# Optimization experiments

Hardware: AMD Instinct MI355X
Metric: run time of the kernel (lower is better)

Reference implementation:

```python
import jax, jax.numpy as jnp
import numpy as np

N = 65536          # nodes
E = N * 7          # edges (avg_degree = n_edge_type = 7)
C_IN = 128
C_OUT = 128
N_EDGE_TYPE = 7
N_NODE_TYPE = 5
FEAT = C_IN + N_NODE_TYPE  # 133, channels after one-hot concat


def setup_inputs() -> dict:
    key = jax.random.key(0)
    k1, k2, k3, k4, k5 = jax.random.split(key, 5)
    x = jax.random.normal(k1, (N, C_IN), dtype=jnp.float32)
    edge_idx = jax.random.randint(k2, (2, E), 0, N, dtype=jnp.int64)
    edge_type = jax.random.randint(k3, (E,), 0, N_EDGE_TYPE, dtype=jnp.int64)
    node_type = jax.random.randint(k4, (N,), 0, N_NODE_TYPE, dtype=jnp.int64)
    # uniform init a la module's reset_parameters
    fan_in = 7 * C_IN
    fan_out = 7 * C_OUT
    a = np.sqrt(3.0) * np.sqrt(2.0 / (fan_in + fan_out))
    weights = jax.random.uniform(k5, (N_EDGE_TYPE * FEAT, C_OUT), dtype=jnp.float32,
                                 minval=-a, maxval=a)
    return {"x": x, "edge_idx": edge_idx, "edge_type": edge_type,
            "node_type": node_type, "weights": weights}


def reference(x, edge_idx, edge_type, node_type, weights):
    # one-hot node type concat (n_node_type > 1 branch)
    one_hot = jax.nn.one_hot(node_type, N_NODE_TYPE, dtype=x.dtype)
    xa = jnp.concatenate([x, one_hot], axis=1)          # [N, FEAT]
    row, col = edge_idx[0], edge_idx[1]
    seg = row * N_EDGE_TYPE + edge_type                 # [E]
    gathered = xa[col]                                  # [E, FEAT]
    num_seg = N * N_EDGE_TYPE
    sums = jax.ops.segment_sum(gathered, seg, num_segments=num_seg)
    cnt = jax.ops.segment_sum(jnp.ones((E,), dtype=xa.dtype), seg, num_segments=num_seg)
    col_data = sums / jnp.maximum(cnt, 1.0)[:, None]    # scatter_mean
    # overwrite self-loop slot (last edge type) with node's own features
    self_idx = jnp.arange(N, dtype=jnp.int64) * N_EDGE_TYPE + (N_EDGE_TYPE - 1)
    col_data = col_data.at[self_idx].set(xa)
    out = col_data.reshape(N, N_EDGE_TYPE * FEAT) @ weights  # [N, C_OUT]
    return out
```

## Files before the change

### kernel.cpp

```cpp
#include <hip/hip_runtime.h>
#include <hip/hip_bf16.h>

#define N_NODES 65536
#define N_EDGES (N_NODES * 7)
#define NSEG    (N_NODES * 7)
#define CAP     12
#define ZROW    65536

typedef short short8 __attribute__((ext_vector_type(8)));
typedef float f32x4  __attribute__((ext_vector_type(4)));

__device__ __forceinline__ unsigned short f2bf(float f) {
    return __builtin_bit_cast(unsigned short, (__bf16)f);
}
__device__ __forceinline__ unsigned pack2(float lo, float hi) {
    return (unsigned)f2bf(lo) | ((unsigned)f2bf(hi) << 16);
}
__device__ __forceinline__ float bflo(unsigned d) { return __uint_as_float(d << 16); }
__device__ __forceinline__ float bfhi(unsigned d) { return __uint_as_float(d & 0xffff0000u); }

__global__ __launch_bounds__(256) void k_big(const float* __restrict__ x,
                                             const int* __restrict__ eidx,
                                             const int* __restrict__ etype,
                                             const int* __restrict__ ntype,
                                             const float* __restrict__ W,
                                             unsigned short* __restrict__ xb,
                                             unsigned short* __restrict__ wb,
                                             unsigned* __restrict__ seg32,
                                             unsigned short* __restrict__ scol) {
    int i = blockIdx.x * 256 + threadIdx.x;

    if (i < N_EDGES) {
        int t = etype[i];
        if (t < 6) {
            int r = eidx[i];
            int c = eidx[N_EDGES + i];
            int u = ntype[c];
            unsigned seg = (unsigned)r * 7u + (unsigned)t;
            unsigned inc = 1u | (1u << (7 + 5 * u));
            unsigned old = atomicAdd(&seg32[seg], inc);
            unsigned slot = old & 0x7fu;
            if (slot < CAP) scol[seg * CAP + slot] = (unsigned short)c;
        }
    }

    {
        int row = i >> 4, mm = i & 15;
        const f32x4* p = reinterpret_cast<const f32x4*>(x + (size_t)row * 128 + mm * 8);
        f32x4 v0 = p[0], v1 = p[1];
        uint4 w;
        w.x = pack2(v0[0], v0[1]); w.y = pack2(v0[2], v0[3]);
        w.z = pack2(v1[0], v1[1]); w.w = pack2(v1[2], v1[3]);
        reinterpret_cast<uint4*>(xb)[i] = w;
    }

    if (i < 16) reinterpret_cast<uint4*>(xb + (size_t)ZROW * 128)[i] = (uint4){0u, 0u, 0u, 0u};

    if (i < 143360) {
        int j    = i & 7;
        int lane = (i >> 3) & 63;
        int cb   = (i >> 9) & 7;
        int tkc  = i >> 12;
        int kc   = tkc % 5;
        int t    = tkc / 5;
        int k = kc * 32 + ((lane >> 4) << 3) + j;
        int c = cb * 16 + (lane & 15);
        float v = (k < 133) ? W[(t * 133 + k) * 128 + c] : 0.0f;
        wb[i] = f2bf(v);
    }
}

__global__ __launch_bounds__(512, 6) void k_main(const unsigned short* __restrict__ xb,
                                                 const int* __restrict__ ntype,
                                                 const unsigned* __restrict__ seg32,
                                                 const unsigned short* __restrict__ scol,
                                                 const unsigned short* __restrict__ wb,
                                                 float* __restrict__ out) {
    __shared__ unsigned short sA[4 * 32 * 168];

    const int tid  = threadIdx.x;
    const int lane = tid & 63;
    const int wid  = tid >> 6;
    const int n0   = blockIdx.x * 32;
    const int r    = tid >> 4;
    const int m    = tid & 15;
    const int n    = n0 + r;

    #pragma unroll
    for (int k2 = 0; k2 < 3; ++k2) {
        int i = tid + k2 * 512;
        int row = i / 12, j = i - row * 12;
        reinterpret_cast<unsigned*>(sA)[row * 84 + 68 + j] = 0u;
    }

    unsigned sv[6], c_t[6];
    uint2 q2[6];
    #pragma unroll
    for (int t = 0; t < 6; ++t) {
        sv[t]  = seg32[n * 7 + t];
        c_t[t] = sv[t] & 0x7fu;
        q2[t]  = *reinterpret_cast<const uint2*>(scol + ((size_t)n * 7 + t) * CAP);
    }

    auto build_tile = [&](int t, int tile, short8 xa, short8 xbv) {
        const unsigned cntv = c_t[t];
        const float inv = (cntv > 1u) ? __builtin_amdgcn_rcpf((float)cntv) : 1.0f;
        uint4 a4 = *reinterpret_cast<const uint4*>(&xa);
        uint4 w;
        if (cntv <= 1u) {
            w = a4;
        } else {
            uint4 b4 = *reinterpret_cast<const uint4*>(&xbv);
            float a[8];
            a[0] = bflo(a4.x) + bflo(b4.x); a[1] = bfhi(a4.x) + bfhi(b4.x);
            a[2] = bflo(a4.y) + bflo(b4.y); a[3] = bfhi(a4.y) + bfhi(b4.y);
            a[4] = bflo(a4.z) + bflo(b4.z); a[5] = bfhi(a4.z) + bfhi(b4.z);
            a[6] = bflo(a4.w) + bflo(b4.w); a[7] = bfhi(a4.w) + bfhi(b4.w);
            if (cntv >= 3u) {
                const unsigned ce = (cntv < (unsigned)CAP) ? cntv : (unsigned)CAP;
                {
                    unsigned c2 = q2[t].y & 0xffffu;
                    short8 v = *reinterpret_cast<const short8*>(xb + (size_t)c2 * 128 + m * 8);
                    uint4 v4 = *reinterpret_cast<const uint4*>(&v);
                    a[0] += bflo(v4.x); a[1] += bfhi(v4.x);
                    a[2] += bflo(v4.y); a[3] += bfhi(v4.y);
                    a[4] += bflo(v4.z); a[5] += bfhi(v4.z);
                    a[6] += bflo(v4.w); a[7] += bfhi(v4.w);
                }
                if (ce >= 4u) {
                    unsigned c3 = q2[t].y >> 16;
                    short8 v = *reinterpret_cast<const short8*>(xb + (size_t)c3 * 128 + m * 8);
                    uint4 v4 = *reinterpret_cast<const uint4*>(&v);
                    a[0] += bflo(v4.x); a[1] += bfhi(v4.x);
                    a[2] += bflo(v4.y); a[3] += bfhi(v4.y);
                    a[4] += bflo(v4.z); a[5] += bfhi(v4.z);
                    a[6] += bflo(v4.w); a[7] += bfhi(v4.w);
                    const size_t segbase = ((size_t)n * 7 + t) * CAP;
                    for (unsigned e = 4; e < ce; ++e) {
                        unsigned c = scol[segbase + e];
                        short8 ve = *reinterpret_cast<const short8*>(xb + (size_t)c * 128 + m * 8);
                        uint4 v4e = *reinterpret_cast<const uint4*>(&ve);
                        a[0] += bflo(v4e.x); a[1] += bfhi(v4e.x);
                        a[2] += bflo(v4e.y); a[3] += bfhi(v4e.y);
                        a[4] += bflo(v4e.z); a[5] += bfhi(v4e.z);
                        a[6] += bflo(v4e.w); a[7] += bfhi(v4e.w);
                    }
                }
            }
            w.x = pack2(a[0] * inv, a[1] * inv); w.y = pack2(a[2] * inv, a[3] * inv);
            w.z = pack2(a[4] * inv, a[5] * inv); w.w = pack2(a[6] * inv, a[7] * inv);
        }
        *reinterpret_cast<uint4*>(sA + (tile * 32 + r) * 168 + m * 8) = w;
        if (m < 4) {
            int i0 = 2 * m, i1 = 2 * m + 1;
            float g0 = (i0 < 5) ? (float)((sv[t] >> (7 + 5 * i0)) & 31u) : 0.f;
            float g1 = (i1 < 5) ? (float)((sv[t] >> (7 + 5 * i1)) & 31u) : 0.f;
            reinterpret_cast<unsigned*>(sA)[(tile * 32 + r) * 84 + 64 + m] =
                pack2(g0 * inv, g1 * inv);
        }
    };

    {
        short8 xA[3], xB[3], xS;
        #pragma unroll
        for (int t = 0; t < 3; ++t) {
            unsigned cA = (c_t[t] >= 1u) ? (q2[t].x & 0xffffu) : (unsigned)ZROW;
            unsigned cB = (c_t[t] >= 2u) ? (q2[t].x >> 16)     : (unsigned)ZROW;
            xA[t] = *reinterpret_cast<const short8*>(xb + (size_t)cA * 128 + m * 8);
            xB[t] = *reinterpret_cast<const short8*>(xb + (size_t)cB * 128 + m * 8);
        }
        xS = *reinterpret_cast<const short8*>(xb + (size_t)n * 128 + m * 8);
        const int ntS = ntype[n];

        #pragma unroll
        for (int t = 0; t < 3; ++t) build_tile(t, t, xA[t], xB[t]);
        *reinterpret_cast<uint4*>(sA + (3 * 32 + r) * 168 + m * 8) =
            *reinterpret_cast<const uint4*>(&xS);
        if (m < 4) {
            float g0 = (ntS == 2 * m) ? 1.f : 0.f;
            float g1 = (ntS == 2 * m + 1) ? 1.f : 0.f;
            reinterpret_cast<unsigned*>(sA)[(3 * 32 + r) * 84 + 64 + m] = pack2(g0, g1);
        }
    }

    __syncthreads();

    f32x4 acc0 = {0.f, 0.f, 0.f, 0.f};
    f32x4 acc1 = {0.f, 0.f, 0.f, 0.f};
    const int ar = lane & 15;
    const int hi = (lane >> 4) << 3;

    #pragma unroll
    for (int i = 0; i < 4; ++i) {
        const int bt = (i == 3) ? 6 : i;
        short8 bv[5];
        #pragma unroll
        for (int kc = 0; kc < 5; ++kc)
            bv[kc] = *reinterpret_cast<const short8*>(
                wb + ((((bt * 5 + kc) * 8 + wid) << 6) + lane) * 8);
        #pragma unroll
        for (int kc = 0; kc < 5; ++kc) {
            short8 a0 = *reinterpret_cast<const short8*>(
                sA + (i * 32 + ar) * 168 + kc * 32 + hi);
            short8 a1 = *reinterpret_cast<const short8*>(
                sA + (i * 32 + 16 + ar) * 168 + kc * 32 + hi);
            acc0 = __builtin_amdgcn_mfma_f32_16x16x32_bf16(a0, bv[kc], acc0, 0, 0, 0);
            acc1 = __builtin_amdgcn_mfma_f32_16x16x32_bf16(a1, bv[kc], acc1, 0, 0, 0);
        }
    }

    __syncthreads();

    {
        short8 xA2[3], xB2[3];
        #pragma unroll
        for (int t = 3; t < 6; ++t) {
            unsigned cA = (c_t[t] >= 1u) ? (q2[t].x & 0xffffu) : (unsigned)ZROW;
            unsigned cB = (c_t[t] >= 2u) ? (q2[t].x >> 16)     : (unsigned)ZROW;
            xA2[t - 3] = *reinterpret_cast<const short8*>(xb + (size_t)cA * 128 + m * 8);
            xB2[t - 3] = *reinterpret_cast<const short8*>(xb + (size_t)cB * 128 + m * 8);
        }
        #pragma unroll
        for (int t = 0; t < 3; ++t) build_tile(t + 3, t, xA2[t], xB2[t]);
    }

    __syncthreads();

    #pragma unroll
    for (int i = 0; i < 3; ++i) {
        const int bt = 3 + i;
        short8 bv[5];
        #pragma unroll
        for (int kc = 0; kc < 5; ++kc)
            bv[kc] = *reinterpret_cast<const short8*>(
                wb + ((((bt * 5 + kc) * 8 + wid) << 6) + lane) * 8);
        #pragma unroll
        for (int kc = 0; kc < 5; ++kc) {
            short8 a0 = *reinterpret_cast<const short8*>(
                sA + (i * 32 + ar) * 168 + kc * 32 + hi);
            short8 a1 = *reinterpret_cast<const short8*>(
                sA + (i * 32 + 16 + ar) * 168 + kc * 32 + hi);
            acc0 = __builtin_amdgcn_mfma_f32_16x16x32_bf16(a0, bv[kc], acc0, 0, 0, 0);
            acc1 = __builtin_amdgcn_mfma_f32_16x16x32_bf16(a1, bv[kc], acc1, 0, 0, 0);
        }
    }

    const int orow = n0 + ((lane >> 4) << 2);
    const int ocol = (wid << 4) + (lane & 15);
    #pragma unroll
    for (int rr = 0; rr < 4; ++rr) {
        out[(size_t)(orow + rr) * 128 + ocol]      = acc0[rr];
        out[(size_t)(orow + 16 + rr) * 128 + ocol] = acc1[rr];
    }
}


extern "C" void kernel_launch(void* const* d_in, const int* in_sizes, int n_in,
                              void* d_out, int out_size, void* d_ws, size_t ws_size,
                              hipStream_t stream) {
    const float* x     = (const float*)d_in[0];
    const int*   eidx  = (const int*)d_in[1];
    const int*   etype = (const int*)d_in[2];
    const int*   ntype = (const int*)d_in[3];
    const float* W     = (const float*)d_in[4];
    float* out = (float*)d_out;

    unsigned short* xb    = (unsigned short*)d_ws;
    unsigned short* wb    = (unsigned short*)((char*)d_ws + 16777472);
    unsigned*       seg32 = (unsigned*)((char*)d_ws + 17064192);
    unsigned short* scol  = (unsigned short*)((char*)d_ws + 18899200);

    hipMemsetAsync(seg32, 0, NSEG * sizeof(unsigned), stream);
    k_big <<<4096,         256, 0, stream>>>(x, eidx, etype, ntype, W, xb, wb, seg32, scol);
    k_main<<<N_NODES / 32, 512, 0, stream>>>(xb, ntype, seg32, scol, wb, out);
}
```

Before: 79.63 us.

## Shrink LDS tile buffer to three slots and split build/MMA into three phases

The shared A-tile buffer shrinks from four 32-row slots to three. The gather/build and MFMA phases are reorganised into three rounds of two or three edge-type tiles each, where the code before used two rounds of four and three. The launch bound is raised to 8 blocks per CU, so the lower LDS and register footprint can allow more resident blocks to hide gather latency. In exchange it adds a third round with extra __syncthreads barriers and shortens each MFMA burst.

New measurement: 80.04 us. Within noise of the previous version (+0.5%).

```diff
diff --git a/kernel.cpp b/kernel.cpp
--- a/kernel.cpp
+++ b/kernel.cpp
@@ -70,13 +70,13 @@
     }
 }
 
-__global__ __launch_bounds__(512, 6) void k_main(const unsigned short* __restrict__ xb,
+__global__ __launch_bounds__(512, 8) void k_main(const unsigned short* __restrict__ xb,
                                                  const int* __restrict__ ntype,
                                                  const unsigned* __restrict__ seg32,
                                                  const unsigned short* __restrict__ scol,
                                                  const unsigned short* __restrict__ wb,
                                                  float* __restrict__ out) {
-    __shared__ unsigned short sA[4 * 32 * 168];
+    __shared__ unsigned short sA[3 * 32 * 168];
 
     const int tid  = threadIdx.x;
     const int lane = tid & 63;
@@ -86,9 +86,7 @@
     const int m    = tid & 15;
     const int n    = n0 + r;
 
-    #pragma unroll
-    for (int k2 = 0; k2 < 3; ++k2) {
-        int i = tid + k2 * 512;
+    for (int i = tid; i < 3 * 32 * 12; i += 512) {
         int row = i / 12, j = i - row * 12;
         reinterpret_cast<unsigned*>(sA)[row * 84 + 68 + j] = 0u;
     }
@@ -160,10 +158,32 @@
         }
     };
 
-    {
-        short8 xA[3], xB[3], xS;
-        #pragma unroll
-        for (int t = 0; t < 3; ++t) {
+    const int ar = lane & 15;
+    const int hi = (lane >> 4) << 3;
+    f32x4 acc0 = {0.f, 0.f, 0.f, 0.f};
+    f32x4 acc1 = {0.f, 0.f, 0.f, 0.f};
+
+    auto marathon = [&](int slot, int bt) {
+        short8 bv[5];
+        #pragma unroll
+        for (int kc = 0; kc < 5; ++kc)
+            bv[kc] = *reinterpret_cast<const short8*>(
+                wb + ((((bt * 5 + kc) * 8 + wid) << 6) + lane) * 8);
+        #pragma unroll
+        for (int kc = 0; kc < 5; ++kc) {
+            short8 a0 = *reinterpret_cast<const short8*>(
+                sA + (slot * 32 + ar) * 168 + kc * 32 + hi);
+            short8 a1 = *reinterpret_cast<const short8*>(
+                sA + (slot * 32 + 16 + ar) * 168 + kc * 32 + hi);
+            acc0 = __builtin_amdgcn_mfma_f32_16x16x32_bf16(a0, bv[kc], acc0, 0, 0, 0);
+            acc1 = __builtin_amdgcn_mfma_f32_16x16x32_bf16(a1, bv[kc], acc1, 0, 0, 0);
+        }
+    };
+
+    {
+        short8 xA[2], xB[2], xS;
+        #pragma unroll
+        for (int t = 0; t < 2; ++t) {
             unsigned cA = (c_t[t] >= 1u) ? (q2[t].x & 0xffffu) : (unsigned)ZROW;
             unsigned cB = (c_t[t] >= 2u) ? (q2[t].x >> 16)     : (unsigned)ZROW;
             xA[t] = *reinterpret_cast<const short8*>(xb + (size_t)cA * 128 + m * 8);
@@ -172,78 +192,50 @@
         xS = *reinterpret_cast<const short8*>(xb + (size_t)n * 128 + m * 8);
         const int ntS = ntype[n];
 
-        #pragma unroll
-        for (int t = 0; t < 3; ++t) build_tile(t, t, xA[t], xB[t]);
-        *reinterpret_cast<uint4*>(sA + (3 * 32 + r) * 168 + m * 8) =
+        build_tile(0, 0, xA[0], xB[0]);
+        build_tile(1, 1, xA[1], xB[1]);
+        *reinterpret_cast<uint4*>(sA + (2 * 32 + r) * 168 + m * 8) =
             *reinterpret_cast<const uint4*>(&xS);
         if (m < 4) {
             float g0 = (ntS == 2 * m) ? 1.f : 0.f;
             float g1 = (ntS == 2 * m + 1) ? 1.f : 0.f;
-            reinterpret_cast<unsigned*>(sA)[(3 * 32 + r) * 84 + 64 + m] = pack2(g0, g1);
-        }
-    }
-
-    __syncthreads();
-
-    f32x4 acc0 = {0.f, 0.f, 0.f, 0.f};
-    f32x4 acc1 = {0.f, 0.f, 0.f, 0.f};
-    const int ar = lane & 15;
-    const int hi = (lane >> 4) << 3;
-
-    #pragma unroll
-    for (int i = 0; i < 4; ++i) {
-        const int bt = (i == 3) ? 6 : i;
-        short8 bv[5];
-        #pragma unroll
-        for (int kc = 0; kc < 5; ++kc)
-            bv[kc] = *reinterpret_cast<const short8*>(
-                wb + ((((bt * 5 + kc) * 8 + wid) << 6) + lane) * 8);
-        #pragma unroll
-        for (int kc = 0; kc < 5; ++kc) {
-            short8 a0 = *reinterpret_cast<const short8*>(
-                sA + (i * 32 + ar) * 168 + kc * 32 + hi);
-            short8 a1 = *reinterpret_cast<const short8*>(
-                sA + (i * 32 + 16 + ar) * 168 + kc * 32 + hi);
-            acc0 = __builtin_amdgcn_mfma_f32_16x16x32_bf16(a0, bv[kc], acc0, 0, 0, 0);
-            acc1 = __builtin_amdgcn_mfma_f32_16x16x32_bf16(a1, bv[kc], acc1, 0, 0, 0);
-        }
-    }
-
-    __syncthreads();
-
-    {
-        short8 xA2[3], xB2[3];
-        #pragma unroll
-        for (int t = 3; t < 6; ++t) {
+            reinterpret_cast<unsigned*>(sA)[(2 * 32 + r) * 84 + 64 + m] = pack2(g0, g1);
+        }
+    }
+    __syncthreads();
+    marathon(0, 0); marathon(1, 1); marathon(2, 6);
+    __syncthreads();
+
+    {
+        short8 xA[2], xB[2];
+        #pragma unroll
+        for (int t = 2; t < 4; ++t) {
             unsigned cA = (c_t[t] >= 1u) ? (q2[t].x & 0xffffu) : (unsigned)ZROW;
             unsigned cB = (c_t[t] >= 2u) ? (q2[t].x >> 16)     : (unsigned)ZROW;
-            xA2[t - 3] = *reinterpret_cast<const short8*>(xb + (size_t)cA * 128 + m * 8);
-            xB2[t - 3] = *reinterpret_cast<const short8*>(xb + (size_t)cB * 128 + m * 8);
-        }
-        #pragma unroll
-        for (int t = 0; t < 3; ++t) build_tile(t + 3, t, xA2[t], xB2[t]);
-    }
-
-    __syncthreads();
-
-    #pragma unroll
-    for (int i = 0; i < 3; ++i) {
-        const int bt = 3 + i;
-        short8 bv[5];
-        #pragma unroll
-        for (int kc = 0; kc < 5; ++kc)
-            bv[kc] = *reinterpret_cast<const short8*>(
-                wb + ((((bt * 5 + kc) * 8 + wid) << 6) + lane) * 8);
-        #pragma unroll
-        for (int kc = 0; kc < 5; ++kc) {
-            short8 a0 = *reinterpret_cast<const short8*>(
-                sA + (i * 32 + ar) * 168 + kc * 32 + hi);
-            short8 a1 = *reinterpret_cast<const short8*>(
-                sA + (i * 32 + 16 + ar) * 168 + kc * 32 + hi);
-            acc0 = __builtin_amdgcn_mfma_f32_16x16x32_bf16(a0, bv[kc], acc0, 0, 0, 0);
-            acc1 = __builtin_amdgcn_mfma_f32_16x16x32_bf16(a1, bv[kc], acc1, 0, 0, 0);
-        }
-    }
+            xA[t - 2] = *reinterpret_cast<const short8*>(xb + (size_t)cA * 128 + m * 8);
+            xB[t - 2] = *reinterpret_cast<const short8*>(xb + (size_t)cB * 128 + m * 8);
+        }
+        build_tile(2, 0, xA[0], xB[0]);
+        build_tile(3, 1, xA[1], xB[1]);
+    }
+    __syncthreads();
+    marathon(0, 2); marathon(1, 3);
+    __syncthreads();
+
+    {
+        short8 xA[2], xB[2];
+        #pragma unroll
+        for (int t = 4; t < 6; ++t) {
+            unsigned cA = (c_t[t] >= 1u) ? (q2[t].x & 0xffffu) : (unsigned)ZROW;
+            unsigned cB = (c_t[t] >= 2u) ? (q2[t].x >> 16)     : (unsigned)ZROW;
+            xA[t - 4] = *reinterpret_cast<const short8*>(xb + (size_t)cA * 128 + m * 8);
+            xB[t - 4] = *reinterpret_cast<const short8*>(xb + (size_t)cB * 128 + m * 8);
+        }
+        build_tile(4, 0, xA[0], xB[0]);
+        build_tile(5, 1, xA[1], xB[1]);
+    }
+    __syncthreads();
+    marathon(0, 4); marathon(1, 5);
 
     const int orow = n0 + ((lane >> 4) << 2);
     const int ocol = (wid << 4) + (lane & 15);
```
